# Optimization experiments

Hardware: AMD Instinct MI355X
Metric: run time of the kernel (lower is better)

## Reference

```python
import jax, jax.numpy as jnp
import numpy as np

BATCH, SEQ, INPUT_SIZE, HIDDEN = 64, 512, 1024, 1024


def setup_inputs() -> dict:
    key = jax.random.key(0)
    k1, k2, k3 = jax.random.split(key, 3)
    bound = 1.0 / np.sqrt(INPUT_SIZE + HIDDEN)  # torch Linear default init bound
    inp = jax.random.normal(k1, (BATCH, SEQ, INPUT_SIZE), dtype=jnp.float32)
    h_0 = jnp.zeros((1, BATCH, HIDDEN), dtype=jnp.float32)
    # W laid out as [input_size + hidden, hidden] so concat([x, h]) @ W matches nn.Linear
    W = jax.random.uniform(k2, (INPUT_SIZE + HIDDEN, HIDDEN), minval=-bound, maxval=bound, dtype=jnp.float32)
    b = jax.random.uniform(k3, (HIDDEN,), minval=-bound, maxval=bound, dtype=jnp.float32)
    return {"input": inp, "h_0": h_0, "W": W, "b": b}


def reference(input, h_0, W, b):
    # Split the combined weight: concat([x, h]) @ W == x @ Wx + h @ Wh
    Wx = W[:INPUT_SIZE]          # [input_size, hidden]
    Wh = W[INPUT_SIZE:]          # [hidden, hidden]
    # Precompute the input projection for all timesteps in one big GEMM.
    x_proj = jnp.einsum('bsi,ih->bsh', input, Wx) + b  # [B, S, H]

    def step(h, xp_t):
        h_new = jnp.tanh(xp_t + h @ Wh)
        return h_new, h_new

    h0 = h_0[0]  # squeeze(0) -> [B, H]
    h_last, out = jax.lax.scan(step, h0, jnp.swapaxes(x_proj, 0, 1))  # out: [S, B, H]
    output_seq = jnp.swapaxes(out, 0, 1)  # [B, S, H]
    h_n = h_last[None]  # [1, B, H]
    return output_seq, h_n
```

## Files before the change

### kernel.cpp

```cpp
#include <hip/hip_runtime.h>
#include <hip/hip_bf16.h>

#define BATCH 64
#define SEQ   512
#define ISZ   1024
#define HID   1024
#define OUTSEQ_ELEMS (BATCH * SEQ * HID)
#define NBG   4
#define NCG   16
#define NBLK  (NBG * NCG)

typedef float f32x4 __attribute__((ext_vector_type(4)));
typedef short bf16x8 __attribute__((ext_vector_type(8)));
typedef unsigned u32x4 __attribute__((ext_vector_type(4)));

__device__ __forceinline__ unsigned short f2bf(float f) {
    union { float f; unsigned u; } v; v.f = f;
    unsigned r = v.u + 0x7fffu + ((v.u >> 16) & 1u);
    return (unsigned short)(r >> 16);
}

__device__ __forceinline__ void exch64(unsigned long long* p, unsigned long long d) {
    unsigned long long old = __hip_atomic_exchange(p, d, __ATOMIC_RELAXED,
                                                   __HIP_MEMORY_SCOPE_AGENT);
    asm volatile("" :: "v"(old));
}

__global__ __launch_bounds__(256)
void xproj_gemm(const float* __restrict__ A, const float* __restrict__ W,
                const float* __restrict__ bias, float* __restrict__ C)
{
    __shared__ __align__(16) unsigned short As[128][72];
    __shared__ __align__(16) unsigned short Bs[128][72];
    const int tid  = threadIdx.x;
    const int lane = tid & 63;
    const int wave = tid >> 6;
    const int m0 = blockIdx.y * 128;
    const int n0 = blockIdx.x * 128;
    const int wm = (wave >> 1) * 64;
    const int wn = (wave & 1) * 64;
    const int l15 = lane & 15;
    const int kq8 = (lane >> 4) * 8;

    f32x4 acc[4][4] = {};

    for (int k0 = 0; k0 < ISZ; k0 += 64) {
        #pragma unroll
        for (int i = 0; i < 8; ++i) {
            int idx = tid + i * 256;
            int row = idx >> 4;
            int kq  = idx & 15;
            float4 v = *reinterpret_cast<const float4*>(
                A + (size_t)(m0 + row) * ISZ + k0 + kq * 4);
            unsigned short* dst = &As[row][kq * 4];
            dst[0] = f2bf(v.x); dst[1] = f2bf(v.y);
            dst[2] = f2bf(v.z); dst[3] = f2bf(v.w);
        }
        #pragma unroll
        for (int i = 0; i < 8; ++i) {
            int idx = tid + i * 256;
            int kk = idx >> 5;
            int nq = idx & 31;
            float4 v = *reinterpret_cast<const float4*>(
                W + (size_t)(k0 + kk) * HID + n0 + nq * 4);
            Bs[nq * 4 + 0][kk] = f2bf(v.x);
            Bs[nq * 4 + 1][kk] = f2bf(v.y);
            Bs[nq * 4 + 2][kk] = f2bf(v.z);
            Bs[nq * 4 + 3][kk] = f2bf(v.w);
        }
        __syncthreads();
        #pragma unroll
        for (int kk = 0; kk < 64; kk += 32) {
            const int krd = kk + kq8;
            bf16x8 a[4], b[4];
            #pragma unroll
            for (int mf = 0; mf < 4; ++mf)
                a[mf] = *reinterpret_cast<const bf16x8*>(&As[wm + mf * 16 + l15][krd]);
            #pragma unroll
            for (int nf = 0; nf < 4; ++nf)
                b[nf] = *reinterpret_cast<const bf16x8*>(&Bs[wn + nf * 16 + l15][krd]);
            #pragma unroll
            for (int mf = 0; mf < 4; ++mf)
                #pragma unroll
                for (int nf = 0; nf < 4; ++nf)
                    acc[mf][nf] = __builtin_amdgcn_mfma_f32_16x16x32_bf16(
                        a[mf], b[nf], acc[mf][nf], 0, 0, 0);
        }
        __syncthreads();
    }

    const int r4 = (lane >> 4) * 4;
    #pragma unroll
    for (int nf = 0; nf < 4; ++nf) {
        int col = n0 + wn + nf * 16 + l15;
        float bv = bias[col];
        #pragma unroll
        for (int mf = 0; mf < 4; ++mf) {
            int row = m0 + wm + mf * 16 + r4;
            #pragma unroll
            for (int r = 0; r < 4; ++r)
                C[(size_t)(row + r) * HID + col] = acc[mf][nf][r] + bv;
        }
    }
}

__global__ __launch_bounds__(256, 1)
void rnn_flow(const float* __restrict__ W, const float* __restrict__ h0,
              float* __restrict__ out,
              unsigned* __restrict__ hb0, unsigned* __restrict__ hb1)
{
    __shared__ __align__(16) unsigned short lds[16 * 1032];
    const int tid  = threadIdx.x;
    const int lane = tid & 63;
    const int wave = tid >> 6;
    const int bg = blockIdx.x >> 4;
    const int cg = blockIdx.x & 15;
    const int b0 = bg * 16;
    const int c0 = cg * 64;
    const int l15 = lane & 15;
    const int kq8 = (lane >> 4) * 8;
    const int q4  = (lane >> 4) * 4;

    {
        int row = tid >> 4;
        int c4  = (tid & 15) * 4;
        float4 v = *reinterpret_cast<const float4*>(
            h0 + (size_t)(b0 + row) * HID + c0 + c4);
        unsigned* base = hb0 + (size_t)(b0 + row) * HID + c0 + c4;
        exch64((unsigned long long*)base,
               (unsigned long long)(unsigned)f2bf(v.x)
             | ((unsigned long long)(unsigned)f2bf(v.y) << 32));
        exch64((unsigned long long*)(base + 2),
               (unsigned long long)(unsigned)f2bf(v.z)
             | ((unsigned long long)(unsigned)f2bf(v.w) << 32));
    }

    bf16x8 bfr[32];
    for (int w = 0; w < 4; ++w) {
        #pragma unroll 4
        for (int p = 0; p < 16; ++p) {
            int k  = p * 64 + (tid >> 2);
            int cc = (tid & 3) * 4;
            float4 v = *reinterpret_cast<const float4*>(
                W + (size_t)(ISZ + k) * HID + c0 + w * 16 + cc);
            lds[(cc + 0) * 1032 + k] = f2bf(v.x);
            lds[(cc + 1) * 1032 + k] = f2bf(v.y);
            lds[(cc + 2) * 1032 + k] = f2bf(v.z);
            lds[(cc + 3) * 1032 + k] = f2bf(v.w);
        }
        __syncthreads();
        if (wave == w) {
            #pragma unroll
            for (int ks = 0; ks < 32; ++ks)
                bfr[ks] = *reinterpret_cast<const bf16x8*>(
                    &lds[l15 * 1032 + ks * 32 + kq8]);
        }
        __syncthreads();
    }

    const int gcol = c0 + wave * 16 + l15;

    float xpv[4];
    #pragma unroll
    for (int j = 0; j < 4; ++j)
        xpv[j] = out[(size_t)(b0 + q4 + j) * (SEQ * HID) + gcol];

    for (int t = 0; t < SEQ; ++t) {
        const unsigned* src = (t & 1) ? hb1 : hb0;
        const unsigned texp = (unsigned)t << 16;
        u32x4 q[16];
        int guard = 0;
        for (;;) {
            #pragma unroll
            for (int p = 0; p < 16; ++p) {
                int idx = tid + p * 256;
                const unsigned* sp = src + (size_t)(b0 + (idx >> 8)) * HID
                                         + (idx & 255) * 4;
                asm volatile("global_load_dwordx4 %0, %1, off sc0 sc1"
                             : "=v"(q[p]) : "v"(sp) : "memory");
            }
            asm volatile("s_waitcnt vmcnt(0)" ::: "memory");
            unsigned bad = 0;
            #pragma unroll
            for (int p = 0; p < 16; ++p) {
                bad |= (q[p][0] ^ texp);
                bad |= (q[p][1] ^ texp);
                bad |= (q[p][2] ^ texp);
                bad |= (q[p][3] ^ texp);
            }
            if (!__any((bad & 0xFFFF0000u) != 0)) break;
            if (++guard > (1 << 14)) break;
        }
        #pragma unroll
        for (int p = 0; p < 16; ++p) {
            int idx = tid + p * 256;
            int row = idx >> 8;
            int cq  = (idx & 255) * 4;
            unsigned long long d =
                  (unsigned long long)(q[p][0] & 0xFFFFu)
                | ((unsigned long long)(q[p][1] & 0xFFFFu) << 16)
                | ((unsigned long long)(q[p][2] & 0xFFFFu) << 32)
                | ((unsigned long long)(q[p][3] & 0xFFFFu) << 48);
            *reinterpret_cast<unsigned long long*>(&lds[row * 1032 + cq]) = d;
        }
        __syncthreads();

        f32x4 ac0 = {}, ac1 = {}, ac2 = {}, ac3 = {};
        #pragma unroll
        for (int g = 0; g < 4; ++g) {
            bf16x8 Af[8];
            #pragma unroll
            for (int m = 0; m < 8; ++m)
                Af[m] = *reinterpret_cast<const bf16x8*>(
                    &lds[l15 * 1032 + (g * 8 + m) * 32 + kq8]);
            ac0 = __builtin_amdgcn_mfma_f32_16x16x32_bf16(Af[0], bfr[g*8+0], ac0, 0, 0, 0);
            ac1 = __builtin_amdgcn_mfma_f32_16x16x32_bf16(Af[1], bfr[g*8+1], ac1, 0, 0, 0);
            ac2 = __builtin_amdgcn_mfma_f32_16x16x32_bf16(Af[2], bfr[g*8+2], ac2, 0, 0, 0);
            ac3 = __builtin_amdgcn_mfma_f32_16x16x32_bf16(Af[3], bfr[g*8+3], ac3, 0, 0, 0);
            ac0 = __builtin_amdgcn_mfma_f32_16x16x32_bf16(Af[4], bfr[g*8+4], ac0, 0, 0, 0);
            ac1 = __builtin_amdgcn_mfma_f32_16x16x32_bf16(Af[5], bfr[g*8+5], ac1, 0, 0, 0);
            ac2 = __builtin_amdgcn_mfma_f32_16x16x32_bf16(Af[6], bfr[g*8+6], ac2, 0, 0, 0);
            ac3 = __builtin_amdgcn_mfma_f32_16x16x32_bf16(Af[7], bfr[g*8+7], ac3, 0, 0, 0);
        }
        __syncthreads();
        f32x4 acc = (ac0 + ac1) + (ac2 + ac3);

        float hv[4];
        #pragma unroll
        for (int j = 0; j < 4; ++j)
            hv[j] = tanhf(acc[j] + xpv[j]);

        if (t < SEQ - 1) {
            unsigned* dst = (t & 1) ? hb0 : hb1;
            const unsigned tagv = (unsigned)(t + 1) << 16;
            #pragma unroll
            for (int j = 0; j < 4; ++j) {
                unsigned e  = tagv | (unsigned)f2bf(hv[j]);
                unsigned pe = __shfl(e, lane | 1);
                if ((lane & 1) == 0) {
                    unsigned long long d = (unsigned long long)e
                                         | ((unsigned long long)pe << 32);
                    exch64((unsigned long long*)(dst
                              + (size_t)(b0 + q4 + j) * HID + gcol), d);
                }
            }
        }

        #pragma unroll
        for (int j = 0; j < 4; ++j)
            out[(size_t)(b0 + q4 + j) * (SEQ * HID) + (size_t)t * HID + gcol] = hv[j];
        if (t == SEQ - 1) {
            #pragma unroll
            for (int j = 0; j < 4; ++j)
                out[(size_t)OUTSEQ_ELEMS + (size_t)(b0 + q4 + j) * HID + gcol] = hv[j];
        } else {
            #pragma unroll
            for (int j = 0; j < 4; ++j)
                xpv[j] = out[(size_t)(b0 + q4 + j) * (SEQ * HID)
                             + (size_t)(t + 1) * HID + gcol];
        }
    }
}

extern "C" void kernel_launch(void* const* d_in, const int* in_sizes, int n_in,
                              void* d_out, int out_size, void* d_ws, size_t ws_size,
                              hipStream_t stream)
{
    const float* input = (const float*)d_in[0];
    const float* h0    = (const float*)d_in[1];
    const float* W     = (const float*)d_in[2];
    const float* bias  = (const float*)d_in[3];
    float* out = (float*)d_out;

    unsigned* hb0 = (unsigned*)d_ws;
    unsigned* hb1 = hb0 + (size_t)BATCH * HID;

    hipMemsetAsync(d_ws, 0xFF, (size_t)2 * BATCH * HID * sizeof(unsigned), stream);

    dim3 gA(HID / 128, (BATCH * SEQ) / 128);
    xproj_gemm<<<gA, dim3(256), 0, stream>>>(input, W, bias, out);

    rnn_flow<<<dim3(NBLK), dim3(256), 0, stream>>>(W, h0, out, hb0, hb1);
}
```

Baseline: 2.613 ms.

## Prefetch next-step hidden state, double-buffer LDS, and use plain coherent stores

Replaces the atomic exchanges that publish hidden-state values with plain global stores carrying sc0/sc1 bits, and issues the next timestep's hidden-state loads right after the stores so they overlap the epilogue. The spin loop now re-polls only the rows that are still stale, and the LDS staging buffer is double-buffered so the trailing barrier after the MFMA loop can be removed. The intent is to shorten the per-step cross-block sync latency. The speculative loads will often see stale tags and need a retry, and plain stores may give different visibility ordering than the atomics did.

```diff
diff --git a/kernel.cpp b/kernel.cpp
--- a/kernel.cpp
+++ b/kernel.cpp
@@ -18,12 +18,6 @@
     union { float f; unsigned u; } v; v.f = f;
     unsigned r = v.u + 0x7fffu + ((v.u >> 16) & 1u);
     return (unsigned short)(r >> 16);
-}
-
-__device__ __forceinline__ void exch64(unsigned long long* p, unsigned long long d) {
-    unsigned long long old = __hip_atomic_exchange(p, d, __ATOMIC_RELAXED,
-                                                   __HIP_MEMORY_SCOPE_AGENT);
-    asm volatile("" :: "v"(old));
 }
 
 __global__ __launch_bounds__(256)
@@ -109,7 +103,7 @@
               float* __restrict__ out,
               unsigned* __restrict__ hb0, unsigned* __restrict__ hb1)
 {
-    __shared__ __align__(16) unsigned short lds[16 * 1032];
+    __shared__ __align__(16) unsigned short lds[2][16 * 1032];
     const int tid  = threadIdx.x;
     const int lane = tid & 63;
     const int wave = tid >> 6;
@@ -126,36 +120,38 @@
         int c4  = (tid & 15) * 4;
         float4 v = *reinterpret_cast<const float4*>(
             h0 + (size_t)(b0 + row) * HID + c0 + c4);
-        unsigned* base = hb0 + (size_t)(b0 + row) * HID + c0 + c4;
-        exch64((unsigned long long*)base,
-               (unsigned long long)(unsigned)f2bf(v.x)
-             | ((unsigned long long)(unsigned)f2bf(v.y) << 32));
-        exch64((unsigned long long*)(base + 2),
-               (unsigned long long)(unsigned)f2bf(v.z)
-             | ((unsigned long long)(unsigned)f2bf(v.w) << 32));
+        u32x4 d;
+        d[0] = (unsigned)f2bf(v.x); d[1] = (unsigned)f2bf(v.y);
+        d[2] = (unsigned)f2bf(v.z); d[3] = (unsigned)f2bf(v.w);
+        unsigned* p = hb0 + (size_t)(b0 + row) * HID + c0 + c4;
+        asm volatile("global_store_dwordx4 %0, %1, off sc0 sc1"
+                     :: "v"(p), "v"(d) : "memory");
     }
 
     bf16x8 bfr[32];
-    for (int w = 0; w < 4; ++w) {
-        #pragma unroll 4
-        for (int p = 0; p < 16; ++p) {
-            int k  = p * 64 + (tid >> 2);
-            int cc = (tid & 3) * 4;
-            float4 v = *reinterpret_cast<const float4*>(
-                W + (size_t)(ISZ + k) * HID + c0 + w * 16 + cc);
-            lds[(cc + 0) * 1032 + k] = f2bf(v.x);
-            lds[(cc + 1) * 1032 + k] = f2bf(v.y);
-            lds[(cc + 2) * 1032 + k] = f2bf(v.z);
-            lds[(cc + 3) * 1032 + k] = f2bf(v.w);
-        }
-        __syncthreads();
-        if (wave == w) {
-            #pragma unroll
-            for (int ks = 0; ks < 32; ++ks)
-                bfr[ks] = *reinterpret_cast<const bf16x8*>(
-                    &lds[l15 * 1032 + ks * 32 + kq8]);
-        }
-        __syncthreads();
+    {
+        unsigned short* l0 = &lds[0][0];
+        for (int w = 0; w < 4; ++w) {
+            #pragma unroll 4
+            for (int p = 0; p < 16; ++p) {
+                int k  = p * 64 + (tid >> 2);
+                int cc = (tid & 3) * 4;
+                float4 v = *reinterpret_cast<const float4*>(
+                    W + (size_t)(ISZ + k) * HID + c0 + w * 16 + cc);
+                l0[(cc + 0) * 1032 + k] = f2bf(v.x);
+                l0[(cc + 1) * 1032 + k] = f2bf(v.y);
+                l0[(cc + 2) * 1032 + k] = f2bf(v.z);
+                l0[(cc + 3) * 1032 + k] = f2bf(v.w);
+            }
+            __syncthreads();
+            if (wave == w) {
+                #pragma unroll
+                for (int ks = 0; ks < 32; ++ks)
+                    bfr[ks] = *reinterpret_cast<const bf16x8*>(
+                        &l0[l15 * 1032 + ks * 32 + kq8]);
+            }
+            __syncthreads();
+        }
     }
 
     const int gcol = c0 + wave * 16 + l15;
@@ -165,43 +161,59 @@
     for (int j = 0; j < 4; ++j)
         xpv[j] = out[(size_t)(b0 + q4 + j) * (SEQ * HID) + gcol];
 
+    u32x4 q[16];
+    #pragma unroll
+    for (int p = 0; p < 16; ++p) {
+        const unsigned* sp = hb0 + (size_t)(b0 + p) * HID + tid * 4;
+        asm volatile("global_load_dwordx4 %0, %1, off sc0 sc1"
+                     : "=v"(q[p]) : "v"(sp) : "memory");
+    }
+
     for (int t = 0; t < SEQ; ++t) {
         const unsigned* src = (t & 1) ? hb1 : hb0;
         const unsigned texp = (unsigned)t << 16;
-        u32x4 q[16];
+
+        asm volatile("s_waitcnt vmcnt(0)" ::: "memory");
+        unsigned stale = 0;
+        #pragma unroll
+        for (int p = 0; p < 16; ++p) {
+            unsigned bad = (q[p][0] ^ texp) | (q[p][1] ^ texp)
+                         | (q[p][2] ^ texp) | (q[p][3] ^ texp);
+            if (bad & 0xFFFF0000u) stale |= (1u << p);
+        }
         int guard = 0;
-        for (;;) {
+        while (stale) {
             #pragma unroll
             for (int p = 0; p < 16; ++p) {
-                int idx = tid + p * 256;
-                const unsigned* sp = src + (size_t)(b0 + (idx >> 8)) * HID
-                                         + (idx & 255) * 4;
-                asm volatile("global_load_dwordx4 %0, %1, off sc0 sc1"
-                             : "=v"(q[p]) : "v"(sp) : "memory");
+                if (stale & (1u << p)) {
+                    const unsigned* sp = src + (size_t)(b0 + p) * HID + tid * 4;
+                    asm volatile("global_load_dwordx4 %0, %1, off sc0 sc1"
+                                 : "=v"(q[p]) : "v"(sp) : "memory");
+                }
             }
             asm volatile("s_waitcnt vmcnt(0)" ::: "memory");
-            unsigned bad = 0;
+            unsigned ns = 0;
             #pragma unroll
             for (int p = 0; p < 16; ++p) {
-                bad |= (q[p][0] ^ texp);
-                bad |= (q[p][1] ^ texp);
-                bad |= (q[p][2] ^ texp);
-                bad |= (q[p][3] ^ texp);
-            }
-            if (!__any((bad & 0xFFFF0000u) != 0)) break;
+                if (stale & (1u << p)) {
+                    unsigned bad = (q[p][0] ^ texp) | (q[p][1] ^ texp)
+                                 | (q[p][2] ^ texp) | (q[p][3] ^ texp);
+                    if (bad & 0xFFFF0000u) ns |= (1u << p);
+                }
+            }
+            stale = ns;
             if (++guard > (1 << 14)) break;
         }
+
+        unsigned short* lb = &lds[t & 1][0];
         #pragma unroll
         for (int p = 0; p < 16; ++p) {
-            int idx = tid + p * 256;
-            int row = idx >> 8;
-            int cq  = (idx & 255) * 4;
             unsigned long long d =
                   (unsigned long long)(q[p][0] & 0xFFFFu)
                 | ((unsigned long long)(q[p][1] & 0xFFFFu) << 16)
                 | ((unsigned long long)(q[p][2] & 0xFFFFu) << 32)
                 | ((unsigned long long)(q[p][3] & 0xFFFFu) << 48);
-            *reinterpret_cast<unsigned long long*>(&lds[row * 1032 + cq]) = d;
+            *reinterpret_cast<unsigned long long*>(&lb[p * 1032 + tid * 4]) = d;
         }
         __syncthreads();
 
@@ -212,7 +224,7 @@
             #pragma unroll
             for (int m = 0; m < 8; ++m)
                 Af[m] = *reinterpret_cast<const bf16x8*>(
-                    &lds[l15 * 1032 + (g * 8 + m) * 32 + kq8]);
+                    &lb[l15 * 1032 + (g * 8 + m) * 32 + kq8]);
             ac0 = __builtin_amdgcn_mfma_f32_16x16x32_bf16(Af[0], bfr[g*8+0], ac0, 0, 0, 0);
             ac1 = __builtin_amdgcn_mfma_f32_16x16x32_bf16(Af[1], bfr[g*8+1], ac1, 0, 0, 0);
             ac2 = __builtin_amdgcn_mfma_f32_16x16x32_bf16(Af[2], bfr[g*8+2], ac2, 0, 0, 0);
@@ -222,7 +234,6 @@
             ac2 = __builtin_amdgcn_mfma_f32_16x16x32_bf16(Af[6], bfr[g*8+6], ac2, 0, 0, 0);
             ac3 = __builtin_amdgcn_mfma_f32_16x16x32_bf16(Af[7], bfr[g*8+7], ac3, 0, 0, 0);
         }
-        __syncthreads();
         f32x4 acc = (ac0 + ac1) + (ac2 + ac3);
 
         float hv[4];
@@ -240,9 +251,16 @@
                 if ((lane & 1) == 0) {
                     unsigned long long d = (unsigned long long)e
                                          | ((unsigned long long)pe << 32);
-                    exch64((unsigned long long*)(dst
-                              + (size_t)(b0 + q4 + j) * HID + gcol), d);
+                    unsigned* p = dst + (size_t)(b0 + q4 + j) * HID + gcol;
+                    asm volatile("global_store_dwordx2 %0, %1, off sc0 sc1"
+                                 :: "v"(p), "v"(d) : "memory");
                 }
+            }
+            #pragma unroll
+            for (int p = 0; p < 16; ++p) {
+                const unsigned* sp = dst + (size_t)(b0 + p) * HID + tid * 4;
+                asm volatile("global_load_dwordx4 %0, %1, off sc0 sc1"
+                             : "=v"(q[p]) : "v"(sp) : "memory");
             }
         }
 
```

Result: faster. 2.264 ms (-13.4%).
